# Optimization experiments

Measured on AMD Instinct MI355X. Metric: run time of the kernel, lower is better.

The kernel has to match this reference:

```python
import jax, jax.numpy as jnp
import numpy as np

NEG_SLOPE = 0.2  # PyG GATv2Conv default negative_slope


def _gatv2(x, src, dst, Wl, Wr, att, bias, N, H, C):
    # GATv2: e_ij = att . leaky_relu(Wl x_j + Wr x_i); segment softmax over dst; scatter-add messages Wl x_j
    xl = (x @ Wl).reshape(N, H, C)  # source-side transform
    xr = (x @ Wr).reshape(N, H, C)  # target-side transform
    g = jax.nn.leaky_relu(xl[src] + xr[dst], NEG_SLOPE)  # [E, H, C]
    e = jnp.einsum('ehc,hc->eh', g, att)                 # [E, H]
    emax = jax.lax.stop_gradient(jax.ops.segment_max(e, dst, num_segments=N))
    p = jnp.exp(e - emax[dst])
    denom = jax.ops.segment_sum(p, dst, num_segments=N)
    alpha = p / denom[dst]                                # segment softmax [E, H]
    out = jax.ops.segment_sum(alpha[:, :, None] * xl[src], dst, num_segments=N)
    return out.reshape(N, H * C) + bias


def setup_inputs() -> dict:
    key = jax.random.key(0)
    N, E, F, H, C, L = 100000, 1000000, 128, 8, 10, 3
    ks = jax.random.split(key, 2 + 4 * L)
    inp = {
        'x': jax.random.normal(ks[0], (N, F), dtype=jnp.float32),
        'edge_index': jax.random.randint(ks[1], (2, E), 0, N, dtype=jnp.int32),
    }
    dims = [F] + [H * C] * (L - 1)
    for l in range(L):
        din = dims[l]
        s = 1.0 / np.sqrt(din)
        inp[f'Wl{l}'] = (jax.random.normal(ks[2 + 4 * l], (din, H * C)) * s).astype(jnp.float32)
        inp[f'Wr{l}'] = (jax.random.normal(ks[3 + 4 * l], (din, H * C)) * s).astype(jnp.float32)
        inp[f'att{l}'] = (jax.random.normal(ks[4 + 4 * l], (H, C)) * (1.0 / np.sqrt(C))).astype(jnp.float32)
        inp[f'b{l}'] = jnp.zeros((H * C,), jnp.float32)
    return inp


def reference(x, edge_index, Wl0, Wr0, att0, b0, Wl1, Wr1, att1, b1, Wl2, Wr2, att2, b2):
    N = x.shape[0]
    H, C = att0.shape
    # add self loops (PyG default add_self_loops=True)
    loops = jnp.arange(N, dtype=edge_index.dtype)
    src = jnp.concatenate([edge_index[0], loops])
    dst = jnp.concatenate([edge_index[1], loops])
    for Wl, Wr, att, b in ((Wl0, Wr0, att0, b0), (Wl1, Wr1, att1, b1), (Wl2, Wr2, att2, b2)):
        x = jax.nn.elu(_gatv2(x, src, dst, Wl, Wr, att, b, N, H, C))
    return x
```

## Files before the change

kernel.cpp:

```cpp
#include <hip/hip_runtime.h>
#include <cfloat>
#include <cmath>

#define HC 80
#define HH 8
#define CC 10

#define GAP(c) ((c) + ((((c) >> 5)) << 2))


__global__ void hist_kernel(const int* __restrict__ dst, int* __restrict__ counts, int E) {
    int i = blockIdx.x * blockDim.x + threadIdx.x;
    int stride = gridDim.x * blockDim.x;
    for (; i < E; i += stride) atomicAdd(&counts[dst[i]], 1);
}

__global__ void scan_kernel(const int* __restrict__ in, int* __restrict__ out, int n) {
    __shared__ int wsum[16];
    __shared__ int carry;
    if (threadIdx.x == 0) carry = 0;
    __syncthreads();
    int lane = threadIdx.x & 63, w = threadIdx.x >> 6;
    for (int base = 0; base < n; base += 1024) {
        int i = base + (int)threadIdx.x;
        int v = (i < n) ? in[i] : 0;
        int s = v;
        #pragma unroll
        for (int off = 1; off < 64; off <<= 1) {
            int t = __shfl_up(s, off, 64);
            if (lane >= off) s += t;
        }
        if (lane == 63) wsum[w] = s;
        __syncthreads();
        if (w == 0) {
            int ws = (lane < 16) ? wsum[lane] : 0;
            int ss = ws;
            #pragma unroll
            for (int off = 1; off < 16; off <<= 1) {
                int t = __shfl_up(ss, off, 64);
                if (lane >= off) ss += t;
            }
            if (lane < 16) wsum[lane] = ss - ws;
        }
        __syncthreads();
        int c = carry;
        if (i < n) out[i] = c + wsum[w] + s - v;
        __syncthreads();
        if (threadIdx.x == 1023) carry = c + wsum[15] + s;
    }
    __syncthreads();
    if (threadIdx.x == 0) out[n] = carry;
}

__global__ void scatter_kernel(const int* __restrict__ src, const int* __restrict__ dst,
                               int* __restrict__ cursor, int* __restrict__ csr, int E) {
    int i = blockIdx.x * blockDim.x + threadIdx.x;
    int stride = gridDim.x * blockDim.x;
    for (; i < E; i += stride) {
        int p = atomicAdd(&cursor[dst[i]], 1);
        csr[p] = src[i];
    }
}


__global__ __launch_bounds__(320) void gemm_big(
    const float* __restrict__ X, const float* __restrict__ Wl, const float* __restrict__ Wr,
    float* __restrict__ Yl, float* __restrict__ Yr, int N, int K)
{
    __shared__ float xs[16 * 140];
    __shared__ float ws[16 * 176];
    const int tid = threadIdx.x;
    const int rt = tid / 20;
    const int cg = tid - rt * 20;
    const int r0 = rt * 8;
    const int c0 = cg * 8;
    const int rG0 = GAP(r0);
    const int cG0 = GAP(c0);
    const int base = blockIdx.x * 128;

    float4 acc[8][2];
    #pragma unroll
    for (int i = 0; i < 8; ++i) {
        acc[i][0] = make_float4(0.f, 0.f, 0.f, 0.f);
        acc[i][1] = make_float4(0.f, 0.f, 0.f, 0.f);
    }

    for (int k0 = 0; k0 < K; k0 += 16) {
        __syncthreads();
        for (int idx = tid; idx < 512; idx += 320) {
            int r = idx >> 2, kc = (idx & 3) << 2;
            int n = base + r; if (n >= N) n = N - 1;
            float4 v = *(const float4*)(X + (size_t)n * K + k0 + kc);
            int rg = GAP(r);
            xs[(kc + 0) * 140 + rg] = v.x;
            xs[(kc + 1) * 140 + rg] = v.y;
            xs[(kc + 2) * 140 + rg] = v.z;
            xs[(kc + 3) * 140 + rg] = v.w;
        }
        {
            int r = rt;
            int c4 = cg * 4;
            float4 v = *(const float4*)(Wl + (size_t)(k0 + r) * HC + c4);
            *(float4*)&ws[r * 176 + GAP(c4)] = v;
            float4 u = *(const float4*)(Wr + (size_t)(k0 + r) * HC + c4);
            *(float4*)&ws[r * 176 + GAP(c4 + 80)] = u;
        }
        __syncthreads();

        #pragma unroll 4
        for (int k = 0; k < 16; ++k) {
            const float* xk = &xs[k * 140 + rG0];
            float4 xa = *(const float4*)(xk);
            float4 xb = *(const float4*)(xk + 4);
            const float* wk = &ws[k * 176 + cG0];
            float4 wa = *(const float4*)(wk);
            float4 wb = *(const float4*)(wk + 4);
            float xv[8] = {xa.x, xa.y, xa.z, xa.w, xb.x, xb.y, xb.z, xb.w};
            #pragma unroll
            for (int i = 0; i < 8; ++i) {
                acc[i][0].x += xv[i] * wa.x;
                acc[i][0].y += xv[i] * wa.y;
                acc[i][0].z += xv[i] * wa.z;
                acc[i][0].w += xv[i] * wa.w;
                acc[i][1].x += xv[i] * wb.x;
                acc[i][1].y += xv[i] * wb.y;
                acc[i][1].z += xv[i] * wb.z;
                acc[i][1].w += xv[i] * wb.w;
            }
        }
    }

    float* Ybase = (cg < 10) ? (Yl + c0) : (Yr + (c0 - 80));
    #pragma unroll
    for (int i = 0; i < 8; ++i) {
        int n = base + r0 + i;
        if (n < N) {
            float* yp = Ybase + (size_t)n * HC;
            *(float4*)yp = acc[i][0];
            *(float4*)(yp + 4) = acc[i][1];
        }
    }
}


__device__ __forceinline__ float edot8(float2 xv, float2 xrv, float2 av) {
    float t0 = xv.x + xrv.x, t1 = xv.y + xrv.y;
    float l0 = 0.6f * t0 + 0.4f * fabsf(t0);
    float l1 = 0.6f * t1 + 0.4f * fabsf(t1);
    float e = l0 * av.x + l1 * av.y;
    e += __shfl_xor(e, 4, 8);
    e += __shfl_xor(e, 2, 8);
    e += __shfl_xor(e, 1, 8);
    return e;
}

__device__ __forceinline__ void upd(float e, float2 xv, float& m, float& s, float2& a) {
    float diff = e - m;
    if (__builtin_expect(diff > 8.0f, 0)) {
        float sc = exp2f(-diff);
        s = s * sc + 1.f;
        a.x = a.x * sc + xv.x;
        a.y = a.y * sc + xv.y;
        m = e;
    } else {
        float p = exp2f(diff);
        s += p;
        a.x += p * xv.x;
        a.y += p * xv.y;
    }
}

__global__ __launch_bounds__(128) void aggregate_kernel(
    const float* __restrict__ xl, const float* __restrict__ xr,
    const int* __restrict__ csr, const int* __restrict__ offsets,
    const float* __restrict__ att, const float* __restrict__ bias,
    float* __restrict__ xout, int N) {
    int wv = threadIdx.x >> 6;
    int lane = threadIdx.x & 63;
    int n = blockIdx.x * 2 + wv;
    if (n >= N) return;
    int h = lane >> 3;
    int q = lane & 7;
    bool active = q < 5;
    int d = h * CC + (active ? 2 * q : 8);
    const float L2E = 1.4426950408889634f;
    float2 av = make_float2(0.f, 0.f);
    if (active) { av = *(const float2*)(att + d); av.x *= L2E; av.y *= L2E; }
    float2 xrv = *(const float2*)(xr + (size_t)n * HC + d);
    int beg = offsets[n], end = offsets[n + 1];

    float2 v0 = *(const float2*)(xl + (size_t)n * HC + d);
    float m0 = edot8(v0, xrv, av);
    float s0 = 1.f; float2 a0 = v0;
    float m1 = -1e30f, s1 = 0.f; float2 a1 = make_float2(0.f, 0.f);

    int i = beg;
    for (; i + 1 < end; i += 2) {
        int i0 = csr[i], i1 = csr[i + 1];
        float2 x0 = *(const float2*)(xl + (size_t)i0 * HC + d);
        float2 x1 = *(const float2*)(xl + (size_t)i1 * HC + d);
        float e0 = edot8(x0, xrv, av);
        float e1 = edot8(x1, xrv, av);
        upd(e0, x0, m0, s0, a0);
        upd(e1, x1, m1, s1, a1);
    }
    if (i < end) {
        int i0 = csr[i];
        float2 x0 = *(const float2*)(xl + (size_t)i0 * HC + d);
        float e0 = edot8(x0, xrv, av);
        upd(e0, x0, m0, s0, a0);
    }
    float M = fmaxf(m0, m1);
    float f0 = exp2f(m0 - M), f1 = exp2f(m1 - M);
    float s = s0 * f0 + s1 * f1;
    float ax = a0.x * f0 + a1.x * f1;
    float ay = a0.y * f0 + a1.y * f1;

    if (active) {
        float2 bv = *(const float2*)(bias + d);
        float o0 = ax / s + bv.x;
        float o1 = ay / s + bv.y;
        o0 = (o0 > 0.f) ? o0 : (__expf(o0) - 1.f);
        o1 = (o1 > 0.f) ? o1 : (__expf(o1) - 1.f);
        *(float2*)(xout + (size_t)n * HC + d) = make_float2(o0, o1);
    }
}

extern "C" void kernel_launch(void* const* d_in, const int* in_sizes, int n_in,
                              void* d_out, int out_size, void* d_ws, size_t ws_size,
                              hipStream_t stream) {
    int N = out_size / HC;
    int E = in_sizes[1] / 2;
    int F = in_sizes[0] / N;

    const float* x   = (const float*)d_in[0];
    const int*   ei  = (const int*)d_in[1];
    const float* Wl[3]  = {(const float*)d_in[2], (const float*)d_in[6],  (const float*)d_in[10]};
    const float* Wr[3]  = {(const float*)d_in[3], (const float*)d_in[7],  (const float*)d_in[11]};
    const float* att[3] = {(const float*)d_in[4], (const float*)d_in[8],  (const float*)d_in[12]};
    const float* bb[3]  = {(const float*)d_in[5], (const float*)d_in[9],  (const float*)d_in[13]};

    size_t NF = (size_t)N * HC;
    float* xl = (float*)d_ws;
    float* xr = xl + NF;
    float* xb = xr + NF;
    int* counts  = (int*)(xb + NF);
    int* offsets = counts + (N + 1);
    int* cursor  = offsets + (N + 1);
    int* csr     = cursor + N;

    const int* srcv = ei;
    const int* dstv = ei + E;

    hipMemsetAsync(counts, 0, (size_t)(N + 1) * sizeof(int), stream);
    hist_kernel<<<1024, 256, 0, stream>>>(dstv, counts, E);
    scan_kernel<<<1, 1024, 0, stream>>>(counts, offsets, N);
    hipMemcpyAsync(cursor, offsets, (size_t)N * sizeof(int), hipMemcpyDeviceToDevice, stream);
    scatter_kernel<<<1024, 256, 0, stream>>>(srcv, dstv, cursor, csr, E);

    for (int l = 0; l < 3; ++l) {
        const float* xin = (l == 0) ? x : xb;
        int K = (l == 0) ? F : HC;
        gemm_big<<<(N + 127) / 128, 320, 0, stream>>>(xin, Wl[l], Wr[l], xl, xr, N, K);
        float* xout = (l == 2) ? (float*)d_out : xb;
        aggregate_kernel<<<(N + 1) / 2, 128, 0, stream>>>(xl, xr, csr, offsets, att[l], bb[l], xout, N);
    }
}
```

Before: 830.8 us.

## Map one thread per node-head in aggregation and remap GEMM thread tiles

The aggregation kernel now gives each thread one (node, head) pair and has it handle all 10 channels in registers. Eight threads cover one node and 32 nodes share a block. This removes the cross-lane shuffle reduction and the 3-of-8 idle lanes per head, and folds the self-loop into the main loop. The cost is divergence: each wave now holds 8 nodes with different degrees, and the two-accumulator interleaving that gave extra instruction-level parallelism is gone. The GEMM kernel also swaps its thread-to-tile mapping so that row tiles vary fastest, which changes its shared-memory access and store patterns.

Result: faster. 737.4 us (-11.2%).

```diff
diff --git a/kernel.cpp b/kernel.cpp
--- a/kernel.cpp
+++ b/kernel.cpp
@@ -70,8 +70,8 @@
     __shared__ float xs[16 * 140];
     __shared__ float ws[16 * 176];
     const int tid = threadIdx.x;
-    const int rt = tid / 20;
-    const int cg = tid - rt * 20;
+    const int rt = tid & 15;
+    const int cg = tid >> 4;
     const int r0 = rt * 8;
     const int c0 = cg * 8;
     const int rG0 = GAP(r0);
@@ -143,86 +143,78 @@
 }
 
 
-__device__ __forceinline__ float edot8(float2 xv, float2 xrv, float2 av) {
-    float t0 = xv.x + xrv.x, t1 = xv.y + xrv.y;
-    float l0 = 0.6f * t0 + 0.4f * fabsf(t0);
-    float l1 = 0.6f * t1 + 0.4f * fabsf(t1);
-    float e = l0 * av.x + l1 * av.y;
-    e += __shfl_xor(e, 4, 8);
-    e += __shfl_xor(e, 2, 8);
-    e += __shfl_xor(e, 1, 8);
-    return e;
-}
-
-__device__ __forceinline__ void upd(float e, float2 xv, float& m, float& s, float2& a) {
-    float diff = e - m;
-    if (__builtin_expect(diff > 8.0f, 0)) {
-        float sc = exp2f(-diff);
-        s = s * sc + 1.f;
-        a.x = a.x * sc + xv.x;
-        a.y = a.y * sc + xv.y;
-        m = e;
-    } else {
-        float p = exp2f(diff);
-        s += p;
-        a.x += p * xv.x;
-        a.y += p * xv.y;
-    }
-}
-
-__global__ __launch_bounds__(128) void aggregate_kernel(
+__global__ __launch_bounds__(256) void aggregate_kernel(
     const float* __restrict__ xl, const float* __restrict__ xr,
     const int* __restrict__ csr, const int* __restrict__ offsets,
     const float* __restrict__ att, const float* __restrict__ bias,
     float* __restrict__ xout, int N) {
-    int wv = threadIdx.x >> 6;
-    int lane = threadIdx.x & 63;
-    int n = blockIdx.x * 2 + wv;
+    const int tid = threadIdx.x;
+    const int g = tid >> 3;
+    const int h = tid & 7;
+    const int n = blockIdx.x * 32 + g;
     if (n >= N) return;
-    int h = lane >> 3;
-    int q = lane & 7;
-    bool active = q < 5;
-    int d = h * CC + (active ? 2 * q : 8);
     const float L2E = 1.4426950408889634f;
-    float2 av = make_float2(0.f, 0.f);
-    if (active) { av = *(const float2*)(att + d); av.x *= L2E; av.y *= L2E; }
-    float2 xrv = *(const float2*)(xr + (size_t)n * HC + d);
-    int beg = offsets[n], end = offsets[n + 1];
-
-    float2 v0 = *(const float2*)(xl + (size_t)n * HC + d);
-    float m0 = edot8(v0, xrv, av);
-    float s0 = 1.f; float2 a0 = v0;
-    float m1 = -1e30f, s1 = 0.f; float2 a1 = make_float2(0.f, 0.f);
-
-    int i = beg;
-    for (; i + 1 < end; i += 2) {
-        int i0 = csr[i], i1 = csr[i + 1];
-        float2 x0 = *(const float2*)(xl + (size_t)i0 * HC + d);
-        float2 x1 = *(const float2*)(xl + (size_t)i1 * HC + d);
-        float e0 = edot8(x0, xrv, av);
-        float e1 = edot8(x1, xrv, av);
-        upd(e0, x0, m0, s0, a0);
-        upd(e1, x1, m1, s1, a1);
-    }
-    if (i < end) {
-        int i0 = csr[i];
-        float2 x0 = *(const float2*)(xl + (size_t)i0 * HC + d);
-        float e0 = edot8(x0, xrv, av);
-        upd(e0, x0, m0, s0, a0);
-    }
-    float M = fmaxf(m0, m1);
-    float f0 = exp2f(m0 - M), f1 = exp2f(m1 - M);
-    float s = s0 * f0 + s1 * f1;
-    float ax = a0.x * f0 + a1.x * f1;
-    float ay = a0.y * f0 + a1.y * f1;
-
-    if (active) {
-        float2 bv = *(const float2*)(bias + d);
-        float o0 = ax / s + bv.x;
-        float o1 = ay / s + bv.y;
+
+    float attv[10], xrv[10];
+    #pragma unroll
+    for (int j = 0; j < 5; ++j) {
+        float2 a = *(const float2*)(att + h * CC + 2 * j);
+        attv[2 * j] = a.x * L2E; attv[2 * j + 1] = a.y * L2E;
+        float2 r = *(const float2*)(xr + (size_t)n * HC + h * CC + 2 * j);
+        xrv[2 * j] = r.x; xrv[2 * j + 1] = r.y;
+    }
+
+    const int beg = offsets[n], end = offsets[n + 1];
+    float m = -1e30f, s = 0.f;
+    float acc[10];
+    #pragma unroll
+    for (int j = 0; j < 10; ++j) acc[j] = 0.f;
+
+    int i = beg - 1;
+    while (__any(i < end)) {
+        if (i < end) {
+            int src = (i < beg) ? n : csr[i];
+            const float* xp = xl + (size_t)src * HC + h * CC;
+            float xv[10];
+            #pragma unroll
+            for (int j = 0; j < 5; ++j) {
+                float2 v = *(const float2*)(xp + 2 * j);
+                xv[2 * j] = v.x; xv[2 * j + 1] = v.y;
+            }
+            float e = 0.f;
+            #pragma unroll
+            for (int j = 0; j < 10; ++j) {
+                float t = xv[j] + xrv[j];
+                float l = 0.6f * t + 0.4f * fabsf(t);
+                e += l * attv[j];
+            }
+            float diff = e - m;
+            if (__builtin_expect(diff > 8.0f, 0)) {
+                float sc = exp2f(-diff);
+                s = s * sc + 1.f;
+                #pragma unroll
+                for (int j = 0; j < 10; ++j) acc[j] = acc[j] * sc + xv[j];
+                m = e;
+            } else {
+                float p = exp2f(diff);
+                s += p;
+                #pragma unroll
+                for (int j = 0; j < 10; ++j) acc[j] += p * xv[j];
+            }
+        }
+        ++i;
+    }
+
+    float inv = 1.f / s;
+    float* op = xout + (size_t)n * HC + h * CC;
+    #pragma unroll
+    for (int j = 0; j < 5; ++j) {
+        float2 b = *(const float2*)(bias + h * CC + 2 * j);
+        float o0 = acc[2 * j] * inv + b.x;
+        float o1 = acc[2 * j + 1] * inv + b.y;
         o0 = (o0 > 0.f) ? o0 : (__expf(o0) - 1.f);
         o1 = (o1 > 0.f) ? o1 : (__expf(o1) - 1.f);
-        *(float2*)(xout + (size_t)n * HC + d) = make_float2(o0, o1);
+        *(float2*)(op + 2 * j) = make_float2(o0, o1);
     }
 }
 
@@ -263,6 +255,6 @@
         int K = (l == 0) ? F : HC;
         gemm_big<<<(N + 127) / 128, 320, 0, stream>>>(xin, Wl[l], Wr[l], xl, xr, N, K);
         float* xout = (l == 2) ? (float*)d_out : xb;
-        aggregate_kernel<<<(N + 1) / 2, 128, 0, stream>>>(xl, xr, csr, offsets, att[l], bb[l], xout, N);
-    }
-}
+        aggregate_kernel<<<(N + 31) / 32, 256, 0, stream>>>(xl, xr, csr, offsets, att[l], bb[l], xout, N);
+    }
+}
```
